# Kernel tuning notes

Measured on AMD Instinct MI355X. Metric: run time of the kernel, lower is better.

The kernel has to match this reference:

```python
import jax, jax.numpy as jnp
import numpy as np

B, S, D = 2, 2048, 1024
H = 16
HD = D // H


def setup_inputs() -> dict:
    key = jax.random.key(0)
    ks = jax.random.split(key, 6)
    X = jax.random.normal(ks[0], (B, S, D), dtype=jnp.float32)
    # Linear weights stored [in, out] so y = x @ W (torch stores transposed).
    sc = 1.0 / np.sqrt(D)
    Wq = jax.random.normal(ks[1], (D, D), dtype=jnp.float32) * sc
    Wk = jax.random.normal(ks[2], (D, D), dtype=jnp.float32) * sc
    Wv = jax.random.normal(ks[3], (D, D), dtype=jnp.float32) * sc
    Wo = jax.random.normal(ks[4], (D, D), dtype=jnp.float32) * sc
    bo = jax.random.normal(ks[5], (D,), dtype=jnp.float32) * 0.01
    return {"X": X, "Wq": Wq, "Wk": Wk, "Wv": Wv, "Wo": Wo, "bo": bo}


def reference(X, Wq, Wk, Wv, Wo, bo):
    b, n, _ = X.shape
    # QKV projections (no bias, qkv_bias=False), reshape to [b, h, n, hd]
    q = (X @ Wq).reshape(b, n, H, HD).transpose(0, 2, 1, 3)
    k = (X @ Wk).reshape(b, n, H, HD).transpose(0, 2, 1, 3)
    v = (X @ Wv).reshape(b, n, H, HD).transpose(0, 2, 1, 3)
    # Unscaled scores (module's scale flag defaults to False)
    scores = jnp.einsum("bhqd,bhkd->bhqk", q, k)
    causal = jnp.triu(jnp.ones((n, n), dtype=bool), k=1)  # True above diagonal
    scores = jnp.where(causal, -jnp.inf, scores)
    attn = jax.nn.softmax(scores, axis=-1)
    # dropout p=0.0 -> identity
    ctx = jnp.einsum("bhqk,bhkd->bqhd", attn, v).reshape(b, n, H * HD)
    return ctx @ Wo + bo
```

## Files before the change

kernel.cpp:

```cpp
#include <hip/hip_runtime.h>
#include <stdint.h>


typedef __attribute__((ext_vector_type(8))) short short8;
typedef __attribute__((ext_vector_type(4))) float floatx4;

#define S_LEN 2048
#define D_DIM 1024
#define NH 16
#define HD 64
#define L2E 1.44269504088896340736f

__device__ __forceinline__ short f2bf(float f) {
    uint32_t u = __builtin_bit_cast(uint32_t, f);
    uint32_t r = u + 0x7fffu + ((u >> 16) & 1u);
    return (short)(r >> 16);
}
__device__ __forceinline__ uint32_t pack2(float a, float b) {
#if __has_builtin(__builtin_amdgcn_cvt_pk_bf16_f32)
    auto v = __builtin_amdgcn_cvt_pk_bf16_f32(a, b);
    uint32_t r; __builtin_memcpy(&r, &v, sizeof(r)); return r;
#else
    return (uint32_t)(uint16_t)f2bf(a) | ((uint32_t)(uint16_t)f2bf(b) << 16);
#endif
}
__device__ __forceinline__ void gll16(const void* g, void* l) {
    __builtin_amdgcn_global_load_lds(
        (const __attribute__((address_space(1))) void*)g,
        (__attribute__((address_space(3))) void*)l, 16, 0, 0);
}

__global__ __launch_bounds__(256) void castx_kernel(const float* __restrict__ X,
                                                    short* __restrict__ Xb) {
    int i = blockIdx.x * 256 + threadIdx.x;
    const float4 v = *(const float4*)(X + (size_t)i * 4);
    uint2 o;
    o.x = pack2(v.x, v.y);
    o.y = pack2(v.z, v.w);
    *(uint2*)(Xb + (size_t)i * 4) = o;
}

__global__ __launch_bounds__(256) void tcast4_kernel(const float* __restrict__ Wq,
                                                     const float* __restrict__ Wk,
                                                     const float* __restrict__ Wv,
                                                     const float* __restrict__ Wo,
                                                     short* __restrict__ WqkvT,
                                                     short* __restrict__ WoT) {
    const int z = blockIdx.z;
    const float* W = (z == 0) ? Wq : (z == 1) ? Wk : (z == 2) ? Wv : Wo;
    short* WT = (z < 3) ? (WqkvT + (size_t)z * 1024 * 1024) : WoT;
    __shared__ float tile[32][33];
    const int bx = blockIdx.x * 32;
    const int by = blockIdx.y * 32;
    const int tx = threadIdx.x, ty = threadIdx.y;
    for (int i = 0; i < 32; i += 8)
        tile[ty + i][tx] = W[(size_t)(bx + ty + i) * D_DIM + by + tx];
    __syncthreads();
    for (int i = 0; i < 32; i += 8)
        WT[(size_t)(by + ty + i) * D_DIM + bx + tx] = f2bf(tile[tx][ty + i]);
}

__global__ __launch_bounds__(512, 6) void gemm_qkv_kernel(const short* __restrict__ Xb,
                                                          const short* __restrict__ WT,
                                                          short* __restrict__ Qb,
                                                          short* __restrict__ Kb,
                                                          short* __restrict__ Vtb) {
    __shared__ __align__(16) short As[2][128 * 32];
    __shared__ __align__(16) short Bs[2][128 * 32];
    const int m0 = blockIdx.x * 128, n0 = blockIdx.y * 128;
    const int tid = threadIdx.x, lane = tid & 63, wave = tid >> 6;
    const int ln = lane & 15, quad = lane >> 4;
    const int mw = (wave & 1) * 64, nw = (wave >> 1) * 32;
    floatx4 acc[4][2] = {};

    const int srow = tid >> 2, ssrc = (tid & 3) ^ (srow & 3);
    const short* Ab = Xb + (size_t)(m0 + srow) * D_DIM + ssrc * 8;
    const short* Bb = WT + (size_t)(n0 + srow) * D_DIM + ssrc * 8;

#define QSTAGE(buf, kk)                                   \
    {                                                     \
        gll16(Ab + (kk) * 32, &As[buf][tid * 8]);         \
        gll16(Bb + (kk) * 32, &Bs[buf][tid * 8]);         \
    }

    QSTAGE(0, 0);
    int cur = 0;
    for (int kk = 0; kk < 32; kk++) {
        if (kk + 1 < 32) {
            QSTAGE(cur ^ 1, kk + 1);
            asm volatile("s_waitcnt vmcnt(2)" ::: "memory");
        } else {
            asm volatile("s_waitcnt vmcnt(0)" ::: "memory");
        }
        __builtin_amdgcn_s_barrier();
        __builtin_amdgcn_sched_barrier(0);
        short8 a[4], b[2];
        for (int i = 0; i < 4; i++) {
            const int row = mw + i * 16 + ln;
            a[i] = *(const short8*)(&As[cur][row * 32 + ((quad ^ (row & 3)) * 8)]);
        }
        for (int j = 0; j < 2; j++) {
            const int row = nw + j * 16 + ln;
            b[j] = *(const short8*)(&Bs[cur][row * 32 + ((quad ^ (row & 3)) * 8)]);
        }
        __builtin_amdgcn_s_setprio(1);
        for (int i = 0; i < 4; i++)
            for (int j = 0; j < 2; j++)
                acc[i][j] = __builtin_amdgcn_mfma_f32_16x16x32_bf16(a[i], b[j], acc[i][j], 0, 0, 0);
        __builtin_amdgcn_s_setprio(0);
        __builtin_amdgcn_sched_barrier(0);
        __builtin_amdgcn_s_barrier();
        __builtin_amdgcn_sched_barrier(0);
        cur ^= 1;
    }
#undef QSTAGE

    const int nsel = n0 >> 10;
    const float qs = (nsel == 0) ? L2E : 1.f;
    short* outB = (nsel == 0) ? Qb : (nsel == 1 ? Kb : Vtb);
    for (int i = 0; i < 4; i++)
        for (int j = 0; j < 2; j++)
            for (int r = 0; r < 4; r++) {
                const int row = m0 + mw + i * 16 + quad * 4 + r;
                const int col = (n0 & 1023) + nw + j * 16 + ln;
                const int bb = row >> 11, s = row & (S_LEN - 1);
                const int h = col >> 6, hd = col & (HD - 1);
                const short v = f2bf(acc[i][j][r] * qs);
                if (nsel < 2)
                    outB[(((size_t)(bb * NH + h)) * S_LEN + s) * HD + hd] = v;
                else
                    outB[(((size_t)(bb * NH + h)) * HD + hd) * S_LEN + s] = v;
            }
}

__global__ __launch_bounds__(512, 6) void gemm_out_kernel(const short* __restrict__ Cb,
                                                          const short* __restrict__ WoT,
                                                          float* __restrict__ out,
                                                          const float* __restrict__ bias) {
    __shared__ __align__(16) short As[2][128 * 32];
    __shared__ __align__(16) short Bs[2][64 * 32];
    const int m0 = blockIdx.x * 128, n0 = blockIdx.y * 64;
    const int tid = threadIdx.x, lane = tid & 63;
    const int ln = lane & 15, quad = lane >> 4;
    const int wave = tid >> 6;
    const int mw = (wave & 3) * 32, nw = (wave >> 2) * 32;
    const bool heavy = (tid < 256);

    floatx4 acc[2][2] = {};

    const int srow = tid >> 2, ssrc = (tid & 3) ^ (srow & 3);
    const int tb = tid & 255;
    const int brow = tb >> 2, bsrc = (tb & 3) ^ (brow & 3);
    const short* Ab = Cb + (size_t)(m0 + srow) * D_DIM + ssrc * 8;
    const short* Bb = WoT + (size_t)(n0 + brow) * D_DIM + bsrc * 8;

#define OSTAGE(buf, kk)                                                \
    {                                                                  \
        gll16(Ab + (kk) * 32, &As[buf][tid * 8]);                      \
        if (heavy) gll16(Bb + (kk) * 32, &Bs[buf][tb * 8]);            \
    }

    OSTAGE(0, 0);
    int cur = 0;
    for (int kk = 0; kk < 32; kk++) {
        if (kk + 1 < 32) {
            OSTAGE(cur ^ 1, kk + 1);
            if (heavy) asm volatile("s_waitcnt vmcnt(2)" ::: "memory");
            else       asm volatile("s_waitcnt vmcnt(1)" ::: "memory");
        } else {
            asm volatile("s_waitcnt vmcnt(0)" ::: "memory");
        }
        __builtin_amdgcn_s_barrier();
        __builtin_amdgcn_sched_barrier(0);
        short8 a[2], b[2];
        for (int i = 0; i < 2; i++) {
            const int row = mw + i * 16 + ln;
            a[i] = *(const short8*)(&As[cur][row * 32 + ((quad ^ (row & 3)) * 8)]);
        }
        for (int j = 0; j < 2; j++) {
            const int row = nw + j * 16 + ln;
            b[j] = *(const short8*)(&Bs[cur][row * 32 + ((quad ^ (row & 3)) * 8)]);
        }
        __builtin_amdgcn_s_setprio(1);
        for (int i = 0; i < 2; i++)
            for (int j = 0; j < 2; j++)
                acc[i][j] = __builtin_amdgcn_mfma_f32_16x16x32_bf16(a[i], b[j], acc[i][j], 0, 0, 0);
        __builtin_amdgcn_s_setprio(0);
        __builtin_amdgcn_sched_barrier(0);
        __builtin_amdgcn_s_barrier();
        __builtin_amdgcn_sched_barrier(0);
        cur ^= 1;
    }
#undef OSTAGE

    for (int i = 0; i < 2; i++)
        for (int j = 0; j < 2; j++)
            for (int r = 0; r < 4; r++) {
                const int row = m0 + mw + i * 16 + quad * 4 + r;
                const int col = n0 + nw + j * 16 + ln;
                out[(size_t)row * D_DIM + col] = acc[i][j][r] + bias[col];
            }
}

__global__ __launch_bounds__(512, 6) void attn_kernel(const short* __restrict__ Q,
                                                      const short* __restrict__ Kg,
                                                      const short* __restrict__ Vt,
                                                      short* __restrict__ ctx,
                                                      float* __restrict__ Opart,
                                                      float* __restrict__ Lpart) {
    __shared__ __align__(16) short Ks[2][64 * 64];
    __shared__ __align__(16) short Vs[2][64 * 64];
    __shared__ __align__(16) short Ps[8][640];

    const int tid = threadIdx.x, wave = tid >> 6, lane = tid & 63;
    const int ln = lane & 15, quad = lane >> 4;

    const int id = blockIdx.x;
    const int bh = (id & 7) + 8 * ((id >> 3) & 3);
    const int t = id >> 5;

    static const unsigned char TASK[24] = {
        0xF0, 0xE1, 0xD0, 0xC1, 0xB0, 0xA1, 0x90, 0x81,
        0xF1, 0xE0, 0xD1, 0xC0, 0xB1, 0xA0, 0x91, 0x80,
        0x02, 0x12, 0x22, 0x32, 0x42, 0x52, 0x62, 0x72};
    const int code = TASK[t];
    const int qt = code >> 4, mode = code & 3;
    const int n = qt + 1, h0 = n >> 1;
    const int kb = 2 * ((mode == 1) ? h0 : 0);
    const int ke = 2 * ((mode == 0) ? h0 : n);
    const int pidx   = (mode == 2) ? -1 : ((qt - 8) * 32 + bh) * 2 + mode;
    const int kmask0 = 2 * qt;
    const int q0 = qt * 128;
    const int bb = bh >> 4, h = bh & 15;
    short* Pw = Ps[wave];

    const short* qrow = Q + ((size_t)bh * S_LEN + q0 + wave * 16 + ln) * HD;
    const short8 qb0 = *(const short8*)(qrow + quad * 8);
    const short8 qb1 = *(const short8*)(qrow + 32 + quad * 8);
    const int q_abs = q0 + wave * 16 + ln;

    const int srow = tid >> 3, spos = tid & 7, ssrc = spos ^ (srow & 7);
    const size_t kbase = (size_t)bh * S_LEN * HD;
    const size_t vbase = (size_t)bh * HD * S_LEN;

    float l_part = 0.f;
    floatx4 o_acc[4] = {};

#define STAGE(buf, kt_)                                                          \
    {                                                                            \
        const int k0s = (kt_) * 64;                                              \
        gll16(Kg + kbase + (size_t)(k0s + srow) * HD + ssrc * 8,                 \
              &Ks[buf][tid * 8]);                                                \
        gll16(Vt + vbase + (size_t)srow * S_LEN + k0s + ssrc * 8,                \
              &Vs[buf][tid * 8]);                                                \
    }

    int cur = 0;
    STAGE(0, kb);
    for (int kt = kb; kt < ke; kt++) {
        if (kt + 1 < ke) {
            STAGE(cur ^ 1, kt + 1);
            asm volatile("s_waitcnt vmcnt(2)" ::: "memory");
        } else {
            asm volatile("s_waitcnt vmcnt(0)" ::: "memory");
        }
        __builtin_amdgcn_s_barrier();
        __builtin_amdgcn_sched_barrier(0);

        const short* Kc = Ks[cur];
        const short* Vc = Vs[cur];

        floatx4 sc4[4];
        __builtin_amdgcn_s_setprio(1);
        for (int nt = 0; nt < 4; nt++) {
            const int row = nt * 16 + ln;
            const short8 ak0 = *(const short8*)(Kc + row * 64 + ((quad ^ (ln & 7)) * 8));
            const short8 ak1 = *(const short8*)(Kc + row * 64 + (((4 + quad) ^ (ln & 7)) * 8));
            floatx4 z = {};
            z = __builtin_amdgcn_mfma_f32_16x16x32_bf16(ak0, qb0, z, 0, 0, 0);
            z = __builtin_amdgcn_mfma_f32_16x16x32_bf16(ak1, qb1, z, 0, 0, 0);
            sc4[nt] = z;
        }
        __builtin_amdgcn_s_setprio(0);

        if (kt >= kmask0) {
            const int k0 = kt * 64;
            for (int nt = 0; nt < 4; nt++)
                for (int r = 0; r < 4; r++)
                    if (k0 + nt * 16 + quad * 4 + r > q_abs) sc4[nt][r] = -1e30f;
        }

        float ls = 0.f;
        for (int nt = 0; nt < 4; nt++)
            for (int r = 0; r < 4; r++) {
                const float e = exp2f(sc4[nt][r]);
                sc4[nt][r] = e; ls += e;
            }
        l_part += ls;

        for (int p = 0; p < 2; p++) {
            uint2 u0, u1;
            u0.x = pack2(sc4[2 * p][0], sc4[2 * p][1]);
            u0.y = pack2(sc4[2 * p][2], sc4[2 * p][3]);
            u1.x = pack2(sc4[2 * p + 1][0], sc4[2 * p + 1][1]);
            u1.y = pack2(sc4[2 * p + 1][2], sc4[2 * p + 1][3]);
            *(uint2*)&Pw[ln * 40 + quad * 4]      = u0;
            *(uint2*)&Pw[ln * 40 + 16 + quad * 4] = u1;
            const short8 bp = *(const short8*)&Pw[ln * 40 + quad * 8];
            __builtin_amdgcn_s_setprio(1);
            for (int dt = 0; dt < 4; dt++) {
                const int row = dt * 16 + ln;
                const short8 av = *(const short8*)(Vc + row * 64 + (((p * 4 + quad) ^ (ln & 7)) * 8));
                o_acc[dt] = __builtin_amdgcn_mfma_f32_16x16x32_bf16(av, bp, o_acc[dt], 0, 0, 0);
            }
            __builtin_amdgcn_s_setprio(0);
        }

        __builtin_amdgcn_sched_barrier(0);
        __builtin_amdgcn_s_barrier();
        __builtin_amdgcn_sched_barrier(0);
        cur ^= 1;
    }
#undef STAGE

    float l_tot = l_part;
    l_tot += __shfl_xor(l_tot, 16, 64);
    l_tot += __shfl_xor(l_tot, 32, 64);

    if (pidx >= 0) {
        float* Ob = Opart + (size_t)pidx * 8192 + (wave * 16 + ln) * 64;
        for (int dt = 0; dt < 4; dt++)
            *(float4*)(Ob + dt * 16 + quad * 4) = *(float4*)&o_acc[dt];
        if (quad == 0) Lpart[(size_t)pidx * 128 + wave * 16 + ln] = l_tot;
    } else {
        const float rl = 1.f / l_tot;
        const int qr = lane >> 2, sg = lane & 3;
        for (int c = 0; c < 2; c++) {
            for (int dd = 0; dd < 2; dd++) {
                const int dt = c * 2 + dd;
                uint2 u;
                u.x = pack2(o_acc[dt][0] * rl, o_acc[dt][1] * rl);
                u.y = pack2(o_acc[dt][2] * rl, o_acc[dt][3] * rl);
                *(uint2*)&Pw[ln * 40 + dd * 16 + quad * 4] = u;
            }
            const short8 v = *(const short8*)&Pw[qr * 40 + sg * 8];
            const int s = q0 + wave * 16 + qr;
            *(short8*)(ctx + ((size_t)bb * S_LEN + s) * D_DIM + h * HD + sg * 8 + c * 32) = v;
        }
    }
}

__global__ __launch_bounds__(256) void combine_kernel(const float* __restrict__ Opart,
                                                      const float* __restrict__ Lpart,
                                                      short* __restrict__ ctx) {
    const int tile = blockIdx.x;
    const int qt = 8 + (tile >> 5), bh = tile & 31;
    const int bb = bh >> 4, h = bh & 15;
    const int p0 = ((qt - 8) * 32 + bh) * 2;
    const float* O0 = Opart + (size_t)p0 * 8192;
    const float* O1 = O0 + 8192;
    const float* l0 = Lpart + (size_t)p0 * 128;
    const float* l1 = l0 + 128;
    for (int e = threadIdx.x; e < 2048; e += 256) {
        const int q = e >> 4, seg = e & 15;
        const float rl = 1.f / (l0[q] + l1[q]);
        const float4 x0 = *(const float4*)(O0 + q * 64 + seg * 4);
        const float4 x1 = *(const float4*)(O1 + q * 64 + seg * 4);
        uint2 u;
        u.x = pack2((x0.x + x1.x) * rl, (x0.y + x1.y) * rl);
        u.y = pack2((x0.z + x1.z) * rl, (x0.w + x1.w) * rl);
        const int s = qt * 128 + q;
        *(uint2*)(ctx + ((size_t)bb * S_LEN + s) * D_DIM + h * HD + seg * 4) = u;
    }
}

extern "C" void kernel_launch(void* const* d_in, const int* in_sizes, int n_in,
                              void* d_out, int out_size, void* d_ws, size_t ws_size,
                              hipStream_t stream) {
    const float* X  = (const float*)d_in[0];
    const float* Wq = (const float*)d_in[1];
    const float* Wk = (const float*)d_in[2];
    const float* Wv = (const float*)d_in[3];
    const float* Wo = (const float*)d_in[4];
    const float* bo = (const float*)d_in[5];
    float* out = (float*)d_out;

    char* ws = (char*)d_ws;
    const size_t MB = 1024 * 1024;
    short* Xb     = (short*)(ws);
    short* WqkvT  = (short*)(ws + 8  * MB);
    short* Qb     = (short*)(ws + 16 * MB);
    short* Kb     = (short*)(ws + 24 * MB);
    short* Vtb    = (short*)(ws + 32 * MB);
    short* ctxb   = (short*)(ws + 40 * MB);
    short* WoT    = (short*)(ws + 48 * MB);
    float* Opart  = (float*)(ws);
    float* Lpart  = (float*)(ws + 50 * MB);

    castx_kernel<<<4096, 256, 0, stream>>>(X, Xb);
    dim3 tg(32, 32, 4), tb(32, 8);
    tcast4_kernel<<<tg, tb, 0, stream>>>(Wq, Wk, Wv, Wo, WqkvT, WoT);

    dim3 gq(32, 24);
    gemm_qkv_kernel<<<gq, 512, 0, stream>>>(Xb, WqkvT, Qb, Kb, Vtb);

    attn_kernel<<<768, 512, 0, stream>>>(Qb, Kb, Vtb, ctxb, Opart, Lpart);
    combine_kernel<<<256, 256, 0, stream>>>(Opart, Lpart, ctxb);

    dim3 go(32, 16);
    gemm_out_kernel<<<go, 512, 0, stream>>>(ctxb, WoT, out, bo);
}
```

Measured before the change: 184.2 us.

## Merge prep kernels, fuse split-KV combine via atomics, shrink GEMM blocks to 256 threads

The X cast and the four weight transpose-casts now run in a single launch. The separate combine kernel is removed: the second attention block to finish a split pair, detected through an atomic counter, merges both partials and writes ctx. Both GEMMs use 4 waves with larger per-wave tiles instead of 8 waves. These changes cut kernel launches and the Opart round trip, at the cost of fences, atomics and more registers per thread.

```diff
diff --git a/kernel.cpp b/kernel.cpp
--- a/kernel.cpp
+++ b/kernel.cpp
@@ -30,37 +30,42 @@
         (__attribute__((address_space(3))) void*)l, 16, 0, 0);
 }
 
-__global__ __launch_bounds__(256) void castx_kernel(const float* __restrict__ X,
-                                                    short* __restrict__ Xb) {
-    int i = blockIdx.x * 256 + threadIdx.x;
-    const float4 v = *(const float4*)(X + (size_t)i * 4);
-    uint2 o;
-    o.x = pack2(v.x, v.y);
-    o.y = pack2(v.z, v.w);
-    *(uint2*)(Xb + (size_t)i * 4) = o;
-}
-
-__global__ __launch_bounds__(256) void tcast4_kernel(const float* __restrict__ Wq,
-                                                     const float* __restrict__ Wk,
-                                                     const float* __restrict__ Wv,
-                                                     const float* __restrict__ Wo,
-                                                     short* __restrict__ WqkvT,
-                                                     short* __restrict__ WoT) {
-    const int z = blockIdx.z;
-    const float* W = (z == 0) ? Wq : (z == 1) ? Wk : (z == 2) ? Wv : Wo;
-    short* WT = (z < 3) ? (WqkvT + (size_t)z * 1024 * 1024) : WoT;
-    __shared__ float tile[32][33];
-    const int bx = blockIdx.x * 32;
-    const int by = blockIdx.y * 32;
-    const int tx = threadIdx.x, ty = threadIdx.y;
-    for (int i = 0; i < 32; i += 8)
-        tile[ty + i][tx] = W[(size_t)(bx + ty + i) * D_DIM + by + tx];
-    __syncthreads();
-    for (int i = 0; i < 32; i += 8)
-        WT[(size_t)(by + ty + i) * D_DIM + bx + tx] = f2bf(tile[tx][ty + i]);
-}
-
-__global__ __launch_bounds__(512, 6) void gemm_qkv_kernel(const short* __restrict__ Xb,
+__global__ __launch_bounds__(256) void prep_kernel(const float* __restrict__ X,
+                                                   const float* __restrict__ Wq,
+                                                   const float* __restrict__ Wk,
+                                                   const float* __restrict__ Wv,
+                                                   const float* __restrict__ Wo,
+                                                   short* __restrict__ Xb,
+                                                   short* __restrict__ WqkvT,
+                                                   short* __restrict__ WoT,
+                                                   int* __restrict__ flags) {
+    const int b = blockIdx.x, tid = threadIdx.x;
+    if (b < 4096) {
+        if (b == 0) flags[tid & 255] = 0;
+        const int i = b * 256 + tid;
+        const float4 v = *(const float4*)(X + (size_t)i * 4);
+        uint2 o;
+        o.x = pack2(v.x, v.y);
+        o.y = pack2(v.z, v.w);
+        *(uint2*)(Xb + (size_t)i * 4) = o;
+    } else {
+        const int b2 = b - 4096;
+        const int z = b2 >> 10, w = b2 & 1023;
+        const float* W = (z == 0) ? Wq : (z == 1) ? Wk : (z == 2) ? Wv : Wo;
+        short* WT = (z < 3) ? (WqkvT + (size_t)z * 1024 * 1024) : WoT;
+        __shared__ float tile[32][33];
+        const int bx = (w & 31) * 32;
+        const int by = (w >> 5) * 32;
+        const int tx = tid & 31, ty = tid >> 5;
+        for (int i = 0; i < 32; i += 8)
+            tile[ty + i][tx] = W[(size_t)(bx + ty + i) * D_DIM + by + tx];
+        __syncthreads();
+        for (int i = 0; i < 32; i += 8)
+            WT[(size_t)(by + ty + i) * D_DIM + bx + tx] = f2bf(tile[tx][ty + i]);
+    }
+}
+
+__global__ __launch_bounds__(256, 3) void gemm_qkv_kernel(const short* __restrict__ Xb,
                                                           const short* __restrict__ WT,
                                                           short* __restrict__ Qb,
                                                           short* __restrict__ Kb,
@@ -70,17 +75,24 @@
     const int m0 = blockIdx.x * 128, n0 = blockIdx.y * 128;
     const int tid = threadIdx.x, lane = tid & 63, wave = tid >> 6;
     const int ln = lane & 15, quad = lane >> 4;
-    const int mw = (wave & 1) * 64, nw = (wave >> 1) * 32;
-    floatx4 acc[4][2] = {};
-
-    const int srow = tid >> 2, ssrc = (tid & 3) ^ (srow & 3);
-    const short* Ab = Xb + (size_t)(m0 + srow) * D_DIM + ssrc * 8;
-    const short* Bb = WT + (size_t)(n0 + srow) * D_DIM + ssrc * 8;
-
-#define QSTAGE(buf, kk)                                   \
-    {                                                     \
-        gll16(Ab + (kk) * 32, &As[buf][tid * 8]);         \
-        gll16(Bb + (kk) * 32, &Bs[buf][tid * 8]);         \
+    const int mw = (wave & 1) * 64, nw = (wave >> 1) * 64;
+    floatx4 acc[4][4] = {};
+
+    const int c0 = tid, c1 = 256 + tid;
+    const int r0 = c0 >> 2, s0 = (c0 & 3) ^ (r0 & 3);
+    const int r1 = c1 >> 2, s1 = (c1 & 3) ^ (r1 & 3);
+    const short* A0 = Xb + (size_t)(m0 + r0) * D_DIM + s0 * 8;
+    const short* A1 = Xb + (size_t)(m0 + r1) * D_DIM + s1 * 8;
+    const short* B0 = WT + (size_t)(n0 + r0) * D_DIM + s0 * 8;
+    const short* B1 = WT + (size_t)(n0 + r1) * D_DIM + s1 * 8;
+
+#define QSTAGE(buf, kk)                                    \
+    {                                                      \
+        const int o = (kk) * 32;                           \
+        gll16(A0 + o, &As[buf][c0 * 8]);                   \
+        gll16(A1 + o, &As[buf][c1 * 8]);                   \
+        gll16(B0 + o, &Bs[buf][c0 * 8]);                   \
+        gll16(B1 + o, &Bs[buf][c1 * 8]);                   \
     }
 
     QSTAGE(0, 0);
@@ -88,24 +100,24 @@
     for (int kk = 0; kk < 32; kk++) {
         if (kk + 1 < 32) {
             QSTAGE(cur ^ 1, kk + 1);
-            asm volatile("s_waitcnt vmcnt(2)" ::: "memory");
+            asm volatile("s_waitcnt vmcnt(4)" ::: "memory");
         } else {
             asm volatile("s_waitcnt vmcnt(0)" ::: "memory");
         }
         __builtin_amdgcn_s_barrier();
         __builtin_amdgcn_sched_barrier(0);
-        short8 a[4], b[2];
+        short8 a[4], b[4];
         for (int i = 0; i < 4; i++) {
             const int row = mw + i * 16 + ln;
             a[i] = *(const short8*)(&As[cur][row * 32 + ((quad ^ (row & 3)) * 8)]);
         }
-        for (int j = 0; j < 2; j++) {
+        for (int j = 0; j < 4; j++) {
             const int row = nw + j * 16 + ln;
             b[j] = *(const short8*)(&Bs[cur][row * 32 + ((quad ^ (row & 3)) * 8)]);
         }
         __builtin_amdgcn_s_setprio(1);
         for (int i = 0; i < 4; i++)
-            for (int j = 0; j < 2; j++)
+            for (int j = 0; j < 4; j++)
                 acc[i][j] = __builtin_amdgcn_mfma_f32_16x16x32_bf16(a[i], b[j], acc[i][j], 0, 0, 0);
         __builtin_amdgcn_s_setprio(0);
         __builtin_amdgcn_sched_barrier(0);
@@ -119,7 +131,7 @@
     const float qs = (nsel == 0) ? L2E : 1.f;
     short* outB = (nsel == 0) ? Qb : (nsel == 1 ? Kb : Vtb);
     for (int i = 0; i < 4; i++)
-        for (int j = 0; j < 2; j++)
+        for (int j = 0; j < 4; j++)
             for (int r = 0; r < 4; r++) {
                 const int row = m0 + mw + i * 16 + quad * 4 + r;
                 const int col = (n0 & 1023) + nw + j * 16 + ln;
@@ -133,7 +145,7 @@
             }
 }
 
-__global__ __launch_bounds__(512, 6) void gemm_out_kernel(const short* __restrict__ Cb,
+__global__ __launch_bounds__(256, 3) void gemm_out_kernel(const short* __restrict__ Cb,
                                                           const short* __restrict__ WoT,
                                                           float* __restrict__ out,
                                                           const float* __restrict__ bias) {
@@ -143,21 +155,23 @@
     const int tid = threadIdx.x, lane = tid & 63;
     const int ln = lane & 15, quad = lane >> 4;
     const int wave = tid >> 6;
-    const int mw = (wave & 3) * 32, nw = (wave >> 2) * 32;
-    const bool heavy = (tid < 256);
-
-    floatx4 acc[2][2] = {};
-
-    const int srow = tid >> 2, ssrc = (tid & 3) ^ (srow & 3);
-    const int tb = tid & 255;
-    const int brow = tb >> 2, bsrc = (tb & 3) ^ (brow & 3);
-    const short* Ab = Cb + (size_t)(m0 + srow) * D_DIM + ssrc * 8;
-    const short* Bb = WoT + (size_t)(n0 + brow) * D_DIM + bsrc * 8;
-
-#define OSTAGE(buf, kk)                                                \
-    {                                                                  \
-        gll16(Ab + (kk) * 32, &As[buf][tid * 8]);                      \
-        if (heavy) gll16(Bb + (kk) * 32, &Bs[buf][tb * 8]);            \
+    const int mw = (wave & 1) * 64, nw = (wave >> 1) * 32;
+
+    floatx4 acc[4][2] = {};
+
+    const int c0 = tid, c1 = 256 + tid;
+    const int r0 = c0 >> 2, s0 = (c0 & 3) ^ (r0 & 3);
+    const int r1 = c1 >> 2, s1 = (c1 & 3) ^ (r1 & 3);
+    const short* A0 = Cb + (size_t)(m0 + r0) * D_DIM + s0 * 8;
+    const short* A1 = Cb + (size_t)(m0 + r1) * D_DIM + s1 * 8;
+    const short* B0 = WoT + (size_t)(n0 + r0) * D_DIM + s0 * 8;
+
+#define OSTAGE(buf, kk)                                    \
+    {                                                      \
+        const int o = (kk) * 32;                           \
+        gll16(A0 + o, &As[buf][c0 * 8]);                   \
+        gll16(A1 + o, &As[buf][c1 * 8]);                   \
+        gll16(B0 + o, &Bs[buf][c0 * 8]);                   \
     }
 
     OSTAGE(0, 0);
@@ -165,15 +179,14 @@
     for (int kk = 0; kk < 32; kk++) {
         if (kk + 1 < 32) {
             OSTAGE(cur ^ 1, kk + 1);
-            if (heavy) asm volatile("s_waitcnt vmcnt(2)" ::: "memory");
-            else       asm volatile("s_waitcnt vmcnt(1)" ::: "memory");
+            asm volatile("s_waitcnt vmcnt(3)" ::: "memory");
         } else {
             asm volatile("s_waitcnt vmcnt(0)" ::: "memory");
         }
         __builtin_amdgcn_s_barrier();
         __builtin_amdgcn_sched_barrier(0);
-        short8 a[2], b[2];
-        for (int i = 0; i < 2; i++) {
+        short8 a[4], b[2];
+        for (int i = 0; i < 4; i++) {
             const int row = mw + i * 16 + ln;
             a[i] = *(const short8*)(&As[cur][row * 32 + ((quad ^ (row & 3)) * 8)]);
         }
@@ -182,7 +195,7 @@
             b[j] = *(const short8*)(&Bs[cur][row * 32 + ((quad ^ (row & 3)) * 8)]);
         }
         __builtin_amdgcn_s_setprio(1);
-        for (int i = 0; i < 2; i++)
+        for (int i = 0; i < 4; i++)
             for (int j = 0; j < 2; j++)
                 acc[i][j] = __builtin_amdgcn_mfma_f32_16x16x32_bf16(a[i], b[j], acc[i][j], 0, 0, 0);
         __builtin_amdgcn_s_setprio(0);
@@ -193,7 +206,7 @@
     }
 #undef OSTAGE
 
-    for (int i = 0; i < 2; i++)
+    for (int i = 0; i < 4; i++)
         for (int j = 0; j < 2; j++)
             for (int r = 0; r < 4; r++) {
                 const int row = m0 + mw + i * 16 + quad * 4 + r;
@@ -207,10 +220,12 @@
                                                       const short* __restrict__ Vt,
                                                       short* __restrict__ ctx,
                                                       float* __restrict__ Opart,
-                                                      float* __restrict__ Lpart) {
+                                                      float* __restrict__ Lpart,
+                                                      int* __restrict__ flags) {
     __shared__ __align__(16) short Ks[2][64 * 64];
     __shared__ __align__(16) short Vs[2][64 * 64];
     __shared__ __align__(16) short Ps[8][640];
+    __shared__ int s_old;
 
     const int tid = threadIdx.x, wave = tid >> 6, lane = tid & 63;
     const int ln = lane & 15, quad = lane >> 4;
@@ -332,6 +347,30 @@
         for (int dt = 0; dt < 4; dt++)
             *(float4*)(Ob + dt * 16 + quad * 4) = *(float4*)&o_acc[dt];
         if (quad == 0) Lpart[(size_t)pidx * 128 + wave * 16 + ln] = l_tot;
+        __threadfence();
+        if (tid == 0) s_old = atomicAdd(&flags[pidx >> 1], 1);
+        __syncthreads();
+        if (s_old == 1) {
+            __threadfence();
+            const int pp = pidx ^ 1;
+            const float* Op = Opart + (size_t)pp * 8192 + (wave * 16 + ln) * 64;
+            const float l_pp = Lpart[(size_t)pp * 128 + wave * 16 + ln];
+            const float rl = 1.f / (l_tot + l_pp);
+            const int qr = lane >> 2, sg = lane & 3;
+            for (int c = 0; c < 2; c++) {
+                for (int dd = 0; dd < 2; dd++) {
+                    const int dt = c * 2 + dd;
+                    const float4 xp = *(const float4*)(Op + dt * 16 + quad * 4);
+                    uint2 u;
+                    u.x = pack2((o_acc[dt][0] + xp.x) * rl, (o_acc[dt][1] + xp.y) * rl);
+                    u.y = pack2((o_acc[dt][2] + xp.z) * rl, (o_acc[dt][3] + xp.w) * rl);
+                    *(uint2*)&Pw[ln * 40 + dd * 16 + quad * 4] = u;
+                }
+                const short8 v = *(const short8*)&Pw[qr * 40 + sg * 8];
+                const int s = q0 + wave * 16 + qr;
+                *(short8*)(ctx + ((size_t)bb * S_LEN + s) * D_DIM + h * HD + sg * 8 + c * 32) = v;
+            }
+        }
     } else {
         const float rl = 1.f / l_tot;
         const int qr = lane >> 2, sg = lane & 3;
@@ -347,30 +386,6 @@
             const int s = q0 + wave * 16 + qr;
             *(short8*)(ctx + ((size_t)bb * S_LEN + s) * D_DIM + h * HD + sg * 8 + c * 32) = v;
         }
-    }
-}
-
-__global__ __launch_bounds__(256) void combine_kernel(const float* __restrict__ Opart,
-                                                      const float* __restrict__ Lpart,
-                                                      short* __restrict__ ctx) {
-    const int tile = blockIdx.x;
-    const int qt = 8 + (tile >> 5), bh = tile & 31;
-    const int bb = bh >> 4, h = bh & 15;
-    const int p0 = ((qt - 8) * 32 + bh) * 2;
-    const float* O0 = Opart + (size_t)p0 * 8192;
-    const float* O1 = O0 + 8192;
-    const float* l0 = Lpart + (size_t)p0 * 128;
-    const float* l1 = l0 + 128;
-    for (int e = threadIdx.x; e < 2048; e += 256) {
-        const int q = e >> 4, seg = e & 15;
-        const float rl = 1.f / (l0[q] + l1[q]);
-        const float4 x0 = *(const float4*)(O0 + q * 64 + seg * 4);
-        const float4 x1 = *(const float4*)(O1 + q * 64 + seg * 4);
-        uint2 u;
-        u.x = pack2((x0.x + x1.x) * rl, (x0.y + x1.y) * rl);
-        u.y = pack2((x0.z + x1.z) * rl, (x0.w + x1.w) * rl);
-        const int s = qt * 128 + q;
-        *(uint2*)(ctx + ((size_t)bb * S_LEN + s) * D_DIM + h * HD + seg * 4) = u;
     }
 }
 
@@ -396,17 +411,15 @@
     short* WoT    = (short*)(ws + 48 * MB);
     float* Opart  = (float*)(ws);
     float* Lpart  = (float*)(ws + 50 * MB);
-
-    castx_kernel<<<4096, 256, 0, stream>>>(X, Xb);
-    dim3 tg(32, 32, 4), tb(32, 8);
-    tcast4_kernel<<<tg, tb, 0, stream>>>(Wq, Wk, Wv, Wo, WqkvT, WoT);
+    int*   flags  = (int*)(ws + 51 * MB);
+
+    prep_kernel<<<8192, 256, 0, stream>>>(X, Wq, Wk, Wv, Wo, Xb, WqkvT, WoT, flags);
 
     dim3 gq(32, 24);
-    gemm_qkv_kernel<<<gq, 512, 0, stream>>>(Xb, WqkvT, Qb, Kb, Vtb);
-
-    attn_kernel<<<768, 512, 0, stream>>>(Qb, Kb, Vtb, ctxb, Opart, Lpart);
-    combine_kernel<<<256, 256, 0, stream>>>(Opart, Lpart, ctxb);
+    gemm_qkv_kernel<<<gq, 256, 0, stream>>>(Xb, WqkvT, Qb, Kb, Vtb);
+
+    attn_kernel<<<768, 512, 0, stream>>>(Qb, Kb, Vtb, ctxb, Opart, Lpart, flags);
 
     dim3 go(32, 16);
-    gemm_out_kernel<<<go, 512, 0, stream>>>(ctxb, WoT, out, bo);
-}
+    gemm_out_kernel<<<go, 256, 0, stream>>>(ctxb, WoT, out, bo);
+}
```

Result: slower. 369.8 us (+100.7%).
